# Kernel optimization log

Hardware: AMD Instinct MI355X
Metric: run time of the kernel (lower is better)

## Reference

```python
import jax, jax.numpy as jnp
import numpy as np

WS = 7          # window size (square)
SS = 3          # shift size
NH = 6          # num heads
EPS = 1e-5      # LayerNorm eps (torch default)


def _ln(x, g, b):
    m = jnp.mean(x, axis=-1, keepdims=True)
    v = jnp.mean(jnp.square(x - m), axis=-1, keepdims=True)
    return (x - m) * jax.lax.rsqrt(v + EPS) * g + b


def _window_partition(x):
    # (B,H,W,C) -> (B*nW, WS*WS, C)
    B, H, W, C = x.shape
    x = x.reshape(B, H // WS, WS, W // WS, WS, C)
    return x.transpose(0, 1, 3, 2, 4, 5).reshape(-1, WS * WS, C)


def _window_reverse(w, B, H, W):
    C = w.shape[-1]
    x = w.reshape(B, H // WS, W // WS, WS, WS, C)
    return x.transpose(0, 1, 3, 2, 4, 5).reshape(B, H, W, C)


def _make_rpi():
    coords = np.stack(np.meshgrid(np.arange(WS), np.arange(WS), indexing='ij'))  # (2,WS,WS)
    cf = coords.reshape(2, -1)
    rel = cf[:, :, None] - cf[:, None, :]            # (2,N,N)
    rel = rel.transpose(1, 2, 0).astype(np.int64)
    rel[..., 0] += WS - 1
    rel[..., 1] += WS - 1
    rel[..., 0] *= 2 * WS - 1
    return rel.sum(-1)                               # (N,N)


def _make_mask(H, W):
    # standard shifted-window attention mask, values in {0, -100}
    img = np.zeros((H, W), dtype=np.float32)
    cnt = 0
    for hs in (slice(0, -WS), slice(-WS, -SS), slice(-SS, None)):
        for ws_ in (slice(0, -WS), slice(-WS, -SS), slice(-SS, None)):
            img[hs, ws_] = cnt
            cnt += 1
    win = img.reshape(H // WS, WS, W // WS, WS).transpose(0, 2, 1, 3).reshape(-1, WS * WS)
    diff = win[:, None, :] - win[:, :, None]
    return np.where(diff != 0, np.float32(-100.0), np.float32(0.0))  # (nW,N,N)


def setup_inputs() -> dict:
    key = jax.random.key(0)
    ks = jax.random.split(key, 8)
    B, H, W, C = 16, 112, 112, 192
    Dh = C * 4
    s = 0.02
    inp = {
        'x': jax.random.normal(ks[0], (B, H, W, C), jnp.float32),
        'mask_matrix': jnp.asarray(_make_mask(H, W)),
        'rpi': jnp.asarray(_make_rpi(), jnp.int32),
        'rpb_table': s * jax.random.normal(ks[1], ((2 * WS - 1) ** 2, NH), jnp.float32),
        'norm1_g': jnp.ones((C,), jnp.float32),
        'norm1_b': jnp.zeros((C,), jnp.float32),
        'qkv_w': s * jax.random.normal(ks[2], (3 * C, C), jnp.float32),
        'qkv_b': jnp.zeros((3 * C,), jnp.float32),
        'proj_w': s * jax.random.normal(ks[3], (C, C), jnp.float32),
        'proj_b': jnp.zeros((C,), jnp.float32),
        'norm2_g': jnp.ones((C,), jnp.float32),
        'norm2_b': jnp.zeros((C,), jnp.float32),
        'fc1_w': s * jax.random.normal(ks[4], (Dh, C), jnp.float32),
        'fc1_b': jnp.zeros((Dh,), jnp.float32),
        'fc2_w': s * jax.random.normal(ks[5], (C, Dh), jnp.float32),
        'fc2_b': jnp.zeros((C,), jnp.float32),
    }
    return inp


def reference(x, mask_matrix, rpi, rpb_table, norm1_g, norm1_b, qkv_w, qkv_b,
              proj_w, proj_b, norm2_g, norm2_b, fc1_w, fc1_b, fc2_w, fc2_b):
    B, H, W, C = x.shape
    N = WS * WS
    hd = C // NH
    scale = hd ** -0.5

    shortcut = x
    xn = _ln(x, norm1_g, norm1_b)
    shifted = jnp.roll(xn, shift=(-SS, -SS), axis=(1, 2))

    xw = _window_partition(shifted)                          # (B_, N, C)
    B_ = xw.shape[0]
    qkv = xw @ qkv_w.T + qkv_b                               # (B_, N, 3C)
    qkv = qkv.reshape(B_, N, 3, NH, hd).transpose(2, 0, 3, 1, 4)
    q, k, v = qkv[0] * scale, qkv[1], qkv[2]                 # (B_, NH, N, hd)

    attn = jnp.einsum('bhnd,bhmd->bhnm', q, k)               # (B_, NH, N, N)
    bias = rpb_table[rpi.reshape(-1)].reshape(N, N, NH).transpose(2, 0, 1)
    attn = attn + bias[None]

    nW = mask_matrix.shape[0]
    attn = attn.reshape(B_ // nW, nW, NH, N, N) + mask_matrix[None, :, None]
    attn = jax.nn.softmax(attn.reshape(B_, NH, N, N), axis=-1)

    out = jnp.einsum('bhnm,bhmd->bhnd', attn, v)             # (B_, NH, N, hd)
    out = out.transpose(0, 2, 1, 3).reshape(B_, N, C)
    out = out @ proj_w.T + proj_b

    shifted = _window_reverse(out, B, H, W)
    xa = jnp.roll(shifted, shift=(SS, SS), axis=(1, 2))
    x = shortcut + xa

    h = _ln(x, norm2_g, norm2_b)
    h = jax.nn.gelu(h @ fc1_w.T + fc1_b, approximate=False)
    h = h @ fc2_w.T + fc2_b
    return x + h
```

## Files before the change

kernel.cpp:

```cpp
#include <hip/hip_runtime.h>
#include <hip/hip_bf16.h>

typedef __hip_bfloat16 bf16;
typedef __attribute__((ext_vector_type(8))) short bh8;
typedef __attribute__((ext_vector_type(4))) short bh4;
typedef __attribute__((ext_vector_type(4))) float f4;

#define TOKENS 200704
#define CDIM   192

__device__ __forceinline__ void gload16(const bf16* g, bf16* l) {
    __builtin_amdgcn_global_load_lds((const __attribute__((address_space(1))) void*)g,
                                     (__attribute__((address_space(3))) void*)l,
                                     16, 0, 0);
}
#define MFMA __builtin_amdgcn_mfma_f32_16x16x32_bf16

__device__ __forceinline__ void stv(float* p, float v) { *p = v; }
__device__ __forceinline__ void stv(bf16* p, float v)  { *p = __float2bfloat16(v); }
__device__ __forceinline__ short f2bs(float v) {
    bf16 h = __float2bfloat16(v); return *(short*)&h;
}

__device__ __forceinline__ int row2tok(int row) {
    int win = row / 49, n = row - win * 49;
    int b = win >> 8, rem = win & 255;
    int hs = (rem >> 4) * 7 + n / 7;
    int wsx = (rem & 15) * 7 + n % 7;
    int hh = hs + 3; if (hh >= 112) hh -= 112;
    int ww = wsx + 3; if (ww >= 112) ww -= 112;
    return (b * 112 + hh) * 112 + ww;
}

__global__ void cvt_all(const float* __restrict__ a, const float* __restrict__ b,
                        const float* __restrict__ c, const float* __restrict__ d,
                        bf16* __restrict__ dst) {
    int i = blockIdx.x * 256 + threadIdx.x;
    if (i >= 442368) return;
    float v;
    if (i < 110592)       v = a[i];
    else if (i < 147456)  v = b[i - 110592];
    else if (i < 294912)  v = c[i - 147456];
    else                  v = d[i - 294912];
    dst[i] = __float2bfloat16(v);
}

__global__ void bmp_kernel(const int* __restrict__ rpi, const float* __restrict__ tab,
                           const float* __restrict__ mask, float* __restrict__ bmp) {
    int idx = blockIdx.x * 256 + threadIdx.x;
    if (idx >= 98304) return;
    int cls = idx / 24576, rem = idx - cls * 24576;
    int h = rem >> 12, qk = rem & 4095;
    int qq = qk >> 6, kk = qk & 63;
    float v;
    if (kk >= 49) v = -1e30f;
    else if (qq >= 49) v = 0.f;
    else {
        int rep = ((cls & 2) ? 240 : 0) + ((cls & 1) ? 15 : 0);
        v = tab[rpi[qq * 49 + kk] * 6 + h] + mask[rep * 2401 + qq * 49 + kk];
    }
    bmp[idx] = v;
}

template<int GATHER>
__global__ __launch_bounds__(256)
void ln_kernel(const float* __restrict__ src, const float* __restrict__ gw,
               const float* __restrict__ bw, bf16* __restrict__ dst) {
    const int lane = threadIdx.x & 63;
    const int gwv  = (blockIdx.x * 256 + threadIdx.x) >> 6;
    const int nwv  = (gridDim.x * 256) >> 6;
    const float g0 = gw[lane], g1 = gw[lane + 64], g2 = gw[lane + 128];
    const float b0 = bw[lane], b1 = bw[lane + 64], b2 = bw[lane + 128];
    for (int row = gwv; row < TOKENS; row += nwv) {
        const float* p = GATHER ? src + (size_t)row2tok(row) * CDIM
                                : src + (size_t)row * CDIM;
        float v0 = p[lane], v1 = p[lane + 64], v2 = p[lane + 128];
        float s = v0 + v1 + v2;
        float q = v0 * v0 + v1 * v1 + v2 * v2;
        #pragma unroll
        for (int o = 32; o; o >>= 1) { s += __shfl_xor(s, o, 64); q += __shfl_xor(q, o, 64); }
        float mean = s * (1.f / 192.f);
        float var  = q * (1.f / 192.f) - mean * mean;
        float rstd = rsqrtf(var + 1e-5f);
        bf16* d = dst + (size_t)row * CDIM;
        d[lane]       = __float2bfloat16((v0 - mean) * rstd * g0 + b0);
        d[lane + 64]  = __float2bfloat16((v1 - mean) * rstd * g1 + b1);
        d[lane + 128] = __float2bfloat16((v2 - mean) * rstd * g2 + b2);
    }
}

template<int EPI, int FUSELN, typename OutT>
__global__ __launch_bounds__(256)
void gemm_bt(const bf16* __restrict__ A, const bf16* __restrict__ W,
             const float* __restrict__ bias, OutT* out,
             const float* res, int N, int K,
             const float* __restrict__ g2, const float* __restrict__ b2g,
             bf16* __restrict__ hbuf) {
    __shared__ __align__(16) bf16 As[128 * 32];
    __shared__ __align__(16) bf16 Bs[192 * 32];
    __shared__ float rsum[FUSELN ? 128 : 1][2], rsq[FUSELN ? 128 : 1][2];
    const int tid = threadIdx.x, wid = tid >> 6, lane = tid & 63;
    const int mbase = blockIdx.y * 128, nbase = blockIdx.x * 192;
    const int wm = wid >> 1, wn = wid & 1;
    const int r = lane & 15, q = lane >> 4;
    const int sx = (q ^ ((r >> 1) & 3)) << 3;
    const bf16* Ab = A + (size_t)mbase * K;
    const bf16* Wb = W + (size_t)nbase * K;
    f4 acc[4][6] = {};
    const int cbase = wid * 64 + lane;
    for (int k0 = 0; k0 < K; k0 += 32) {
        #pragma unroll
        for (int p = 0; p < 2; ++p) {
            int ci = p * 256 + cbase;
            int row = ci >> 2, g = (ci & 3) ^ ((row >> 1) & 3);
            gload16(Ab + (size_t)row * K + (k0 + (g << 3)),
                    &As[(p * 256 + wid * 64) * 8]);
        }
        #pragma unroll
        for (int p = 0; p < 3; ++p) {
            int ci = p * 256 + cbase;
            int row = ci >> 2, g = (ci & 3) ^ ((row >> 1) & 3);
            gload16(Wb + (size_t)row * K + (k0 + (g << 3)),
                    &Bs[(p * 256 + wid * 64) * 8]);
        }
        __syncthreads();
        bh8 af[4], bfr[6];
        #pragma unroll
        for (int i = 0; i < 4; ++i)
            af[i] = *(const bh8*)&As[(wm * 64 + i * 16 + r) * 32 + sx];
        #pragma unroll
        for (int j = 0; j < 6; ++j)
            bfr[j] = *(const bh8*)&Bs[(wn * 96 + j * 16 + r) * 32 + sx];
        #pragma unroll
        for (int i = 0; i < 4; ++i)
            #pragma unroll
            for (int j = 0; j < 6; ++j)
                acc[i][j] = MFMA(af[i], bfr[j], acc[i][j], 0, 0, 0);
        __syncthreads();
    }
    const int cr = q, cc = r;
    if constexpr (EPI == 0) {
        #pragma unroll
        for (int i = 0; i < 4; ++i)
            #pragma unroll
            for (int j = 0; j < 6; ++j) {
                int ncol = nbase + wn * 96 + j * 16 + cc;
                float bv = bias[ncol];
                #pragma unroll
                for (int rr = 0; rr < 4; ++rr) {
                    int row = mbase + wm * 64 + i * 16 + cr * 4 + rr;
                    stv(&out[(size_t)row * N + ncol], acc[i][j][rr] + bv);
                }
            }
    } else {
        #pragma unroll
        for (int i = 0; i < 4; ++i) {
            size_t dstRow[4];
            float ps[4], pq[4];
            #pragma unroll
            for (int rr = 0; rr < 4; ++rr) {
                int row = mbase + wm * 64 + i * 16 + cr * 4 + rr;
                dstRow[rr] = (size_t)row2tok(row) * CDIM;
                ps[rr] = 0.f; pq[rr] = 0.f;
            }
            #pragma unroll
            for (int j = 0; j < 6; ++j) {
                int ncol = nbase + wn * 96 + j * 16 + cc;
                float bv = bias[ncol];
                #pragma unroll
                for (int rr = 0; rr < 4; ++rr) {
                    float v = acc[i][j][rr] + bv + res[dstRow[rr] + ncol];
                    stv(&out[dstRow[rr] + ncol], v);
                    acc[i][j][rr] = v;
                    ps[rr] += v; pq[rr] += v * v;
                }
            }
            if constexpr (FUSELN) {
                #pragma unroll
                for (int rr = 0; rr < 4; ++rr) {
                    float s = ps[rr], qq = pq[rr];
                    #pragma unroll
                    for (int o = 1; o < 16; o <<= 1) { s += __shfl_xor(s, o, 64); qq += __shfl_xor(qq, o, 64); }
                    if (cc == 0) {
                        int rl = wm * 64 + i * 16 + cr * 4 + rr;
                        rsum[rl][wn] = s; rsq[rl][wn] = qq;
                    }
                }
            }
        }
        if constexpr (FUSELN) {
            __syncthreads();
            #pragma unroll
            for (int i = 0; i < 4; ++i) {
                size_t dstRow[4];
                float mean[4], rstd[4];
                #pragma unroll
                for (int rr = 0; rr < 4; ++rr) {
                    int rl = wm * 64 + i * 16 + cr * 4 + rr;
                    dstRow[rr] = (size_t)row2tok(mbase + rl) * CDIM;
                    float m = (rsum[rl][0] + rsum[rl][1]) * (1.f / 192.f);
                    float var = (rsq[rl][0] + rsq[rl][1]) * (1.f / 192.f) - m * m;
                    mean[rr] = m; rstd[rr] = rsqrtf(var + 1e-5f);
                }
                #pragma unroll
                for (int j = 0; j < 6; ++j) {
                    int ncol = nbase + wn * 96 + j * 16 + cc;
                    float gv = g2[ncol], bvv = b2g[ncol];
                    #pragma unroll
                    for (int rr = 0; rr < 4; ++rr)
                        hbuf[dstRow[rr] + ncol] =
                            __float2bfloat16((acc[i][j][rr] - mean[rr]) * rstd[rr] * gv + bvv);
                }
            }
        }
    }
}

__global__ __launch_bounds__(384, 3)
void qkvattn_kernel(const bf16* __restrict__ xw, const bf16* __restrict__ wq,
                    const float* __restrict__ qkvb, const float* __restrict__ bmp,
                    bf16* __restrict__ attno) {
    __shared__ __align__(16) bf16 xs[2][64][32];
    __shared__ __align__(16) bf16 qk[6][2][64][32];
    __shared__ __align__(16) bf16 vt[6][32][64];
    const int tid = threadIdx.x, h = tid >> 6, lane = tid & 63;
    const int r = lane & 15, q = lane >> 4;
    const int win = blockIdx.x;
    const int sxk = (q ^ ((r >> 1) & 3)) << 3;

    f4 aqk[4][4] = {}, av[4][2] = {};
    if (tid < 256) {
        int tok = tid >> 2, kg = (tid & 3) ^ ((tok >> 1) & 3);
        int srow = win * 49 + tok; if (srow > 200703) srow = 200703;
        gload16(xw + (size_t)srow * 192 + kg * 8, &xs[0][0][0] + tid * 8);
    }
    __syncthreads();
    for (int ks = 0; ks < 6; ++ks) {
        const int buf = ks & 1;
        if (ks < 5 && tid < 256) {
            int tok = tid >> 2, kg = (tid & 3) ^ ((tok >> 1) & 3);
            int srow = win * 49 + tok; if (srow > 200703) srow = 200703;
            gload16(xw + (size_t)srow * 192 + (ks + 1) * 32 + kg * 8,
                    &xs[buf ^ 1][0][0] + tid * 8);
        }
        bh8 wqk[4], wv[2], xf[4];
        #pragma unroll
        for (int i = 0; i < 4; ++i)
            wqk[i] = *(const bh8*)&wq[(size_t)((i >> 1) * 192 + h * 32 + (i & 1) * 16 + r) * 192 + ks * 32 + q * 8];
        #pragma unroll
        for (int jv = 0; jv < 2; ++jv)
            wv[jv] = *(const bh8*)&wq[(size_t)(384 + h * 32 + jv * 16 + r) * 192 + ks * 32 + q * 8];
        #pragma unroll
        for (int mt = 0; mt < 4; ++mt)
            xf[mt] = *(const bh8*)&xs[buf][mt * 16 + r][sxk];
        #pragma unroll
        for (int i = 0; i < 4; ++i)
            #pragma unroll
            for (int jn = 0; jn < 4; ++jn)
                aqk[i][jn] = MFMA(wqk[i], xf[jn], aqk[i][jn], 0, 0, 0);
        #pragma unroll
        for (int mt = 0; mt < 4; ++mt)
            #pragma unroll
            for (int jv = 0; jv < 2; ++jv)
                av[mt][jv] = MFMA(xf[mt], wv[jv], av[mt][jv], 0, 0, 0);
        __syncthreads();
    }
    bf16* qkh = &qk[h][0][0][0];
    #pragma unroll
    for (int i = 0; i < 4; ++i) {
        const int t = i >> 1;
        const f4 bz = *(const f4*)&qkvb[t * 192 + h * 32 + (i & 1) * 16 + q * 4];
        const float sc = (i < 2) ? 0.17677669529663689f : 1.0f;
        #pragma unroll
        for (int jn = 0; jn < 4; ++jn) {
            const int tok = jn * 16 + r;
            bh4 w;
            #pragma unroll
            for (int rr = 0; rr < 4; ++rr)
                w[rr] = f2bs((aqk[i][jn][rr] + bz[rr]) * sc);
            const int g = (((i & 1) * 4 + q) ^ ((tok & 3) << 1));
            *(bh4*)&qkh[(t * 64 + tok) * 32 + g * 4] = w;
        }
    }
    bf16* vth = &vt[h][0][0];
    #pragma unroll
    for (int jv = 0; jv < 2; ++jv) {
        const float bv = qkvb[384 + h * 32 + jv * 16 + r];
        const int d = jv * 16 + r;
        #pragma unroll
        for (int mt = 0; mt < 4; ++mt) {
            bh4 w;
            #pragma unroll
            for (int rr = 0; rr < 4; ++rr)
                w[rr] = f2bs(av[mt][jv][rr] + bv);
            const int g = ((mt * 4 + q) ^ ((r & 7) << 1));
            *(bh4*)&vth[d * 64 + g * 4] = w;
        }
    }
    f4 as[4][4] = {};
    {
        const int sl = ((2 * q) ^ ((r & 3) << 1)) << 2;
        bh8 kf[4], qf[4];
        #pragma unroll
        for (int mt = 0; mt < 4; ++mt)
            kf[mt] = *(const bh8*)&qkh[(64 + mt * 16 + r) * 32 + sl];
        #pragma unroll
        for (int jn = 0; jn < 4; ++jn)
            qf[jn] = *(const bh8*)&qkh[(jn * 16 + r) * 32 + sl];
        #pragma unroll
        for (int mt = 0; mt < 4; ++mt)
            #pragma unroll
            for (int jn = 0; jn < 4; ++jn)
                as[mt][jn] = MFMA(kf[mt], qf[jn], as[mt][jn], 0, 0, 0);
    }
    const int rem = win & 255;
    const int cls = (((rem >> 4) == 15) ? 2 : 0) + (((rem & 15) == 15) ? 1 : 0);
    const float* bmh = bmp + ((size_t)(cls * 6 + h) << 12);
    #pragma unroll
    for (int jn = 0; jn < 4; ++jn) {
        const int qq = jn * 16 + r;
        #pragma unroll
        for (int mt = 0; mt < 4; ++mt) {
            const f4 b = *(const f4*)&bmh[qq * 64 + mt * 16 + q * 4];
            #pragma unroll
            for (int rr = 0; rr < 4; ++rr) as[mt][jn][rr] += b[rr];
        }
    }
    float inv4[4];
    #pragma unroll
    for (int jn = 0; jn < 4; ++jn) {
        float mx = -1e30f;
        #pragma unroll
        for (int mt = 0; mt < 4; ++mt)
            #pragma unroll
            for (int rr = 0; rr < 4; ++rr) mx = fmaxf(mx, as[mt][jn][rr]);
        mx = fmaxf(mx, __shfl_xor(mx, 16, 64));
        mx = fmaxf(mx, __shfl_xor(mx, 32, 64));
        float sm = 0.f;
        #pragma unroll
        for (int mt = 0; mt < 4; ++mt)
            #pragma unroll
            for (int rr = 0; rr < 4; ++rr) {
                float e = __expf(as[mt][jn][rr] - mx);
                as[mt][jn][rr] = e; sm += e;
            }
        sm += __shfl_xor(sm, 16, 64);
        sm += __shfl_xor(sm, 32, 64);
        inv4[jn] = 1.f / sm;
    }
    #pragma unroll
    for (int jn = 0; jn < 4; ++jn) {
        const int qq = jn * 16 + r;
        #pragma unroll
        for (int mt = 0; mt < 4; ++mt) {
            bh4 w;
            #pragma unroll
            for (int rr = 0; rr < 4; ++rr) w[rr] = f2bs(as[mt][jn][rr] * inv4[jn]);
            const int g = ((mt * 4 + q) ^ ((r & 7) << 1));
            *(bh4*)&qkh[qq * 64 + g * 4] = w;
        }
    }
    f4 ao[4][2] = {};
    #pragma unroll
    for (int k2 = 0; k2 < 2; ++k2) {
        const int sl = ((k2 * 8 + 2 * q) ^ ((r & 7) << 1)) << 2;
        bh8 pf[4], vf[2];
        #pragma unroll
        for (int mt = 0; mt < 4; ++mt)
            pf[mt] = *(const bh8*)&qkh[(mt * 16 + r) * 64 + sl];
        #pragma unroll
        for (int jv = 0; jv < 2; ++jv)
            vf[jv] = *(const bh8*)&vth[(jv * 16 + r) * 64 + sl];
        #pragma unroll
        for (int mt = 0; mt < 4; ++mt)
            #pragma unroll
            for (int jv = 0; jv < 2; ++jv)
                ao[mt][jv] = MFMA(pf[mt], vf[jv], ao[mt][jv], 0, 0, 0);
    }
    #pragma unroll
    for (int mt = 0; mt < 4; ++mt)
        #pragma unroll
        for (int jv = 0; jv < 2; ++jv) {
            const int d = jv * 16 + r;
            #pragma unroll
            for (int rr = 0; rr < 4; ++rr) {
                const int qq = mt * 16 + q * 4 + rr;
                if (qq < 49)
                    attno[((size_t)win * 49 + qq) * 192 + h * 32 + d] =
                        __float2bfloat16(ao[mt][jv][rr]);
            }
        }
}

__global__ __launch_bounds__(256, 4)
void mlp_kernel(const bf16* __restrict__ Aht, const bf16* __restrict__ w1,
                const float* __restrict__ b1, const bf16* __restrict__ w2,
                const float* __restrict__ b2, float* __restrict__ out) {
    __shared__ __align__(16) bf16 As[6][64][32];
    __shared__ __align__(16) bf16 Hs[2][64][64];
    const int tid = threadIdx.x, wid = tid >> 6, lane = tid & 63;
    const int mbase = blockIdx.x * 64;
    const int r = lane & 15, q = lane >> 4, ko = q * 8;
    const int sxA = (q ^ ((r >> 1) & 3)) << 3;
    #pragma unroll
    for (int it = 0; it < 6; ++it) {
        int l = it * 256 + wid * 64 + lane;
        int ks = l >> 8, rem2 = l & 255, row = rem2 >> 2;
        int g = (rem2 & 3) ^ ((row >> 1) & 3);
        gload16(Aht + (size_t)(mbase + row) * 192 + ks * 32 + g * 8,
                &As[0][0][0] + (size_t)(it * 256 + wid * 64) * 8);
    }
    __syncthreads();
    f4 acc2[4][3] = {};
    for (int c = 0; c < 12; ++c) {
        const int cb = c * 64;
        bh8 w1f[6];
        #pragma unroll
        for (int ks = 0; ks < 6; ++ks)
            w1f[ks] = *(const bh8*)&w1[(size_t)(cb + wid * 16 + r) * 192 + ks * 32 + ko];
        f4 acc1[4] = {};
        #pragma unroll
        for (int ks = 0; ks < 6; ++ks)
            #pragma unroll
            for (int i = 0; i < 4; ++i) {
                bh8 af = *(const bh8*)(&As[ks][0][0] + (i * 16 + r) * 32 + sxA);
                acc1[i] = MFMA(af, w1f[ks], acc1[i], 0, 0, 0);
            }
        bh8 w2f[2][3];
        #pragma unroll
        for (int k2 = 0; k2 < 2; ++k2)
            #pragma unroll
            for (int j = 0; j < 3; ++j)
                w2f[k2][j] = *(const bh8*)&w2[(size_t)(wid * 48 + j * 16 + r) * 768 + cb + k2 * 32 + ko];
        const float b1v = b1[cb + wid * 16 + r];
        bf16 (*Hp)[64] = Hs[c & 1];
        #pragma unroll
        for (int i = 0; i < 4; ++i) {
            #pragma unroll
            for (int rr = 0; rr < 4; ++rr) {
                int row = i * 16 + q * 4 + rr;
                int col = wid * 16 + r;
                float v = acc1[i][rr] + b1v;
                float u = v * (1.5957691216f + 0.0713548162f * v * v);
                float e = __expf(u);
                Hp[row][(((col >> 3) ^ (row & 7)) << 3) | (col & 7)] =
                    __float2bfloat16(v * e / (e + 1.f));
            }
        }
        __syncthreads();
        #pragma unroll
        for (int k2 = 0; k2 < 2; ++k2)
            #pragma unroll
            for (int i = 0; i < 4; ++i) {
                int row = i * 16 + r;
                bh8 af = *(const bh8*)(&Hp[row][0] + ((((k2 * 4 + q) ^ (row & 7)) & 7) << 3));
                #pragma unroll
                for (int j = 0; j < 3; ++j)
                    acc2[i][j] = MFMA(af, w2f[k2][j], acc2[i][j], 0, 0, 0);
            }
    }
    #pragma unroll
    for (int i = 0; i < 4; ++i)
        #pragma unroll
        for (int j = 0; j < 3; ++j) {
            int ncol = wid * 48 + j * 16 + r;
            float bv = b2[ncol];
            #pragma unroll
            for (int rr = 0; rr < 4; ++rr) {
                size_t idx = (size_t)(mbase + i * 16 + q * 4 + rr) * 192 + ncol;
                out[idx] = acc2[i][j][rr] + bv + out[idx];
            }
        }
}

extern "C" void kernel_launch(void* const* d_in, const int* in_sizes, int n_in,
                              void* d_out, int out_size, void* d_ws, size_t ws_size,
                              hipStream_t stream) {
    const float* x     = (const float*)d_in[0];
    const float* mask  = (const float*)d_in[1];
    const int*   rpi   = (const int*)d_in[2];
    const float* rpb   = (const float*)d_in[3];
    const float* n1g   = (const float*)d_in[4];
    const float* n1b   = (const float*)d_in[5];
    const float* qkvw  = (const float*)d_in[6];
    const float* qkvb  = (const float*)d_in[7];
    const float* projw = (const float*)d_in[8];
    const float* projb = (const float*)d_in[9];
    const float* n2g   = (const float*)d_in[10];
    const float* n2b   = (const float*)d_in[11];
    const float* fc1w  = (const float*)d_in[12];
    const float* fc1b  = (const float*)d_in[13];
    const float* fc2w  = (const float*)d_in[14];
    const float* fc2b  = (const float*)d_in[15];

    char* ws = (char*)d_ws;
    bf16*  attno  = (bf16*)ws;
    float* bmp    = (float*)(ws + 77070336);
    bf16*  wq     = (bf16*)(ws + 77463552);
    bf16*  wp     = (bf16*)(ws + 77684736);
    bf16*  w1     = (bf16*)(ws + 77758464);
    bf16*  w2     = (bf16*)(ws + 78053376);
    bf16*  xw     = (bf16*)d_out;
    float* x1     = (float*)d_out;

    const bool fuse = ws_size >= 155418624ull;
    bf16* hbuf = fuse ? (bf16*)(ws + 78348288) : (bf16*)ws;

    cvt_all<<<1728, 256, 0, stream>>>(qkvw, projw, fc1w, fc2w, wq);
    bmp_kernel<<<384, 256, 0, stream>>>(rpi, rpb, mask, bmp);

    ln_kernel<1><<<2048, 256, 0, stream>>>(x, n1g, n1b, xw);
    qkvattn_kernel<<<4096, 384, 0, stream>>>(xw, wq, qkvb, bmp, attno);
    if (fuse) {
        gemm_bt<1, 1, float><<<dim3(1, 1568), 256, 0, stream>>>(
            attno, wp, projb, x1, x, 192, 192, n2g, n2b, hbuf);
    } else {
        gemm_bt<1, 0, float><<<dim3(1, 1568), 256, 0, stream>>>(
            attno, wp, projb, x1, x, 192, 192, nullptr, nullptr, nullptr);
        ln_kernel<0><<<2048, 256, 0, stream>>>(x1, n2g, n2b, hbuf);
    }
    mlp_kernel<<<3136, 256, 0, stream>>>(hbuf, w1, fc1b, w2, fc2b, (float*)d_out);
}
```

Measured before the change: 737.0 us.

## Fuse output projection, residual add and LayerNorm2 into the attention kernel

```diff
diff --git a/kernel.cpp b/kernel.cpp
--- a/kernel.cpp
+++ b/kernel.cpp
@@ -89,16 +89,13 @@
     }
 }
 
-template<int EPI, int FUSELN, typename OutT>
+template<int EPI, typename OutT>
 __global__ __launch_bounds__(256)
 void gemm_bt(const bf16* __restrict__ A, const bf16* __restrict__ W,
              const float* __restrict__ bias, OutT* out,
-             const float* res, int N, int K,
-             const float* __restrict__ g2, const float* __restrict__ b2g,
-             bf16* __restrict__ hbuf) {
+             const float* res, int N, int K) {
     __shared__ __align__(16) bf16 As[128 * 32];
     __shared__ __align__(16) bf16 Bs[192 * 32];
-    __shared__ float rsum[FUSELN ? 128 : 1][2], rsq[FUSELN ? 128 : 1][2];
     const int tid = threadIdx.x, wid = tid >> 6, lane = tid & 63;
     const int mbase = blockIdx.y * 128, nbase = blockIdx.x * 192;
     const int wm = wid >> 1, wn = wid & 1;
@@ -139,87 +136,38 @@
         __syncthreads();
     }
     const int cr = q, cc = r;
-    if constexpr (EPI == 0) {
-        #pragma unroll
-        for (int i = 0; i < 4; ++i)
-            #pragma unroll
-            for (int j = 0; j < 6; ++j) {
-                int ncol = nbase + wn * 96 + j * 16 + cc;
-                float bv = bias[ncol];
-                #pragma unroll
-                for (int rr = 0; rr < 4; ++rr) {
-                    int row = mbase + wm * 64 + i * 16 + cr * 4 + rr;
-                    stv(&out[(size_t)row * N + ncol], acc[i][j][rr] + bv);
-                }
-            }
-    } else {
-        #pragma unroll
-        for (int i = 0; i < 4; ++i) {
-            size_t dstRow[4];
-            float ps[4], pq[4];
+    #pragma unroll
+    for (int i = 0; i < 4; ++i) {
+        size_t dstRow[4];
+        #pragma unroll
+        for (int rr = 0; rr < 4; ++rr) {
+            int row = mbase + wm * 64 + i * 16 + cr * 4 + rr;
+            dstRow[rr] = (EPI == 1) ? (size_t)row2tok(row) * CDIM : (size_t)row * N;
+        }
+        #pragma unroll
+        for (int j = 0; j < 6; ++j) {
+            int ncol = nbase + wn * 96 + j * 16 + cc;
+            float bv = bias[ncol];
             #pragma unroll
             for (int rr = 0; rr < 4; ++rr) {
-                int row = mbase + wm * 64 + i * 16 + cr * 4 + rr;
-                dstRow[rr] = (size_t)row2tok(row) * CDIM;
-                ps[rr] = 0.f; pq[rr] = 0.f;
-            }
-            #pragma unroll
-            for (int j = 0; j < 6; ++j) {
-                int ncol = nbase + wn * 96 + j * 16 + cc;
-                float bv = bias[ncol];
-                #pragma unroll
-                for (int rr = 0; rr < 4; ++rr) {
-                    float v = acc[i][j][rr] + bv + res[dstRow[rr] + ncol];
-                    stv(&out[dstRow[rr] + ncol], v);
-                    acc[i][j][rr] = v;
-                    ps[rr] += v; pq[rr] += v * v;
-                }
-            }
-            if constexpr (FUSELN) {
-                #pragma unroll
-                for (int rr = 0; rr < 4; ++rr) {
-                    float s = ps[rr], qq = pq[rr];
-                    #pragma unroll
-                    for (int o = 1; o < 16; o <<= 1) { s += __shfl_xor(s, o, 64); qq += __shfl_xor(qq, o, 64); }
-                    if (cc == 0) {
-                        int rl = wm * 64 + i * 16 + cr * 4 + rr;
-                        rsum[rl][wn] = s; rsq[rl][wn] = qq;
-                    }
-                }
-            }
-        }
-        if constexpr (FUSELN) {
-            __syncthreads();
-            #pragma unroll
-            for (int i = 0; i < 4; ++i) {
-                size_t dstRow[4];
-                float mean[4], rstd[4];
-                #pragma unroll
-                for (int rr = 0; rr < 4; ++rr) {
-                    int rl = wm * 64 + i * 16 + cr * 4 + rr;
-                    dstRow[rr] = (size_t)row2tok(mbase + rl) * CDIM;
-                    float m = (rsum[rl][0] + rsum[rl][1]) * (1.f / 192.f);
-                    float var = (rsq[rl][0] + rsq[rl][1]) * (1.f / 192.f) - m * m;
-                    mean[rr] = m; rstd[rr] = rsqrtf(var + 1e-5f);
-                }
-                #pragma unroll
-                for (int j = 0; j < 6; ++j) {
-                    int ncol = nbase + wn * 96 + j * 16 + cc;
-                    float gv = g2[ncol], bvv = b2g[ncol];
-                    #pragma unroll
-                    for (int rr = 0; rr < 4; ++rr)
-                        hbuf[dstRow[rr] + ncol] =
-                            __float2bfloat16((acc[i][j][rr] - mean[rr]) * rstd[rr] * gv + bvv);
-                }
-            }
-        }
-    }
-}
-
+                float v = acc[i][j][rr] + bv;
+                size_t di = dstRow[rr] + ncol;
+                if constexpr (EPI == 1) v += res[di];
+                stv(&out[di], v);
+            }
+        }
+    }
+}
+
+template<int PROJ>
 __global__ __launch_bounds__(384, 3)
 void qkvattn_kernel(const bf16* __restrict__ xw, const bf16* __restrict__ wq,
                     const float* __restrict__ qkvb, const float* __restrict__ bmp,
-                    bf16* __restrict__ attno) {
+                    bf16* __restrict__ attno,
+                    const bf16* __restrict__ wp, const float* __restrict__ projb,
+                    const float* __restrict__ xres, float* __restrict__ x1,
+                    const float* __restrict__ g2, const float* __restrict__ b2g,
+                    bf16* __restrict__ hbuf) {
     __shared__ __align__(16) bf16 xs[2][64][32];
     __shared__ __align__(16) bf16 qk[6][2][64][32];
     __shared__ __align__(16) bf16 vt[6][32][64];
@@ -346,7 +294,7 @@
             }
         sm += __shfl_xor(sm, 16, 64);
         sm += __shfl_xor(sm, 32, 64);
-        inv4[jn] = 1.f / sm;
+        inv4[jn] = __builtin_amdgcn_rcpf(sm);
     }
     #pragma unroll
     for (int jn = 0; jn < 4; ++jn) {
@@ -377,19 +325,126 @@
             for (int jv = 0; jv < 2; ++jv)
                 ao[mt][jv] = MFMA(pf[mt], vf[jv], ao[mt][jv], 0, 0, 0);
     }
+    if constexpr (!PROJ) {
+        #pragma unroll
+        for (int mt = 0; mt < 4; ++mt)
+            #pragma unroll
+            for (int jv = 0; jv < 2; ++jv) {
+                const int d = jv * 16 + r;
+                #pragma unroll
+                for (int rr = 0; rr < 4; ++rr) {
+                    const int qq = mt * 16 + q * 4 + rr;
+                    if (qq < 49)
+                        attno[((size_t)win * 49 + qq) * 192 + h * 32 + d] =
+                            __float2bfloat16(ao[mt][jv][rr]);
+                }
+            }
+        return;
+    } else {
+    __syncthreads();
+    bf16* Os = &qk[0][0][0][0];
+    #pragma unroll
+    for (int jv = 0; jv < 2; ++jv) {
+        const int col = h * 32 + jv * 16 + r;
+        const int gc = col >> 3, cl = col & 7;
+        #pragma unroll
+        for (int mt = 0; mt < 4; ++mt)
+            #pragma unroll
+            for (int rr = 0; rr < 4; ++rr) {
+                const int row = mt * 16 + q * 4 + rr;
+                Os[row * 192 + ((gc ^ ((row >> 1) & 3)) << 3) + cl] =
+                    __float2bfloat16(ao[mt][jv][rr]);
+            }
+    }
+    __syncthreads();
+    f4 pr[4][2] = {};
+    #pragma unroll
+    for (int ks = 0; ks < 6; ++ks) {
+        bh8 wpf[2];
+        #pragma unroll
+        for (int jv = 0; jv < 2; ++jv)
+            wpf[jv] = *(const bh8*)&wp[(size_t)(h * 32 + jv * 16 + r) * 192 + ks * 32 + q * 8];
+        const int kg = ks * 4 + q;
+        #pragma unroll
+        for (int mt = 0; mt < 4; ++mt) {
+            const int row = mt * 16 + r;
+            bh8 of = *(const bh8*)&Os[row * 192 + ((kg ^ ((row >> 1) & 3)) << 3)];
+            #pragma unroll
+            for (int jv = 0; jv < 2; ++jv)
+                pr[mt][jv] = MFMA(of, wpf[jv], pr[mt][jv], 0, 0, 0);
+        }
+    }
+    float pbv[2], g2v[2], b2v[2];
+    #pragma unroll
+    for (int jv = 0; jv < 2; ++jv) {
+        const int col = h * 32 + jv * 16 + r;
+        pbv[jv] = projb[col]; g2v[jv] = g2[col]; b2v[jv] = b2g[col];
+    }
+    int tokm[4][4];
     #pragma unroll
     for (int mt = 0; mt < 4; ++mt)
         #pragma unroll
+        for (int rr = 0; rr < 4; ++rr) {
+            int grow = win * 49 + mt * 16 + q * 4 + rr;
+            if (grow > 200703) grow = 200703;
+            tokm[mt][rr] = row2tok(grow);
+        }
+    #pragma unroll
+    for (int mt = 0; mt < 4; ++mt)
+        #pragma unroll
         for (int jv = 0; jv < 2; ++jv) {
-            const int d = jv * 16 + r;
+            const int col = h * 32 + jv * 16 + r;
             #pragma unroll
             for (int rr = 0; rr < 4; ++rr) {
                 const int qq = mt * 16 + q * 4 + rr;
-                if (qq < 49)
-                    attno[((size_t)win * 49 + qq) * 192 + h * 32 + d] =
-                        __float2bfloat16(ao[mt][jv][rr]);
-            }
-        }
+                const size_t di = (size_t)tokm[mt][rr] * 192 + col;
+                float v = pr[mt][jv][rr] + pbv[jv] + xres[di];
+                pr[mt][jv][rr] = v;
+                if (qq < 49) x1[di] = v;
+            }
+        }
+    float* rs = (float*)&xs[0][0][0];
+    float* rq = rs + 512;
+    float* mr = rs + 1024;
+    #pragma unroll
+    for (int mt = 0; mt < 4; ++mt)
+        #pragma unroll
+        for (int rr = 0; rr < 4; ++rr) {
+            float s = pr[mt][0][rr] + pr[mt][1][rr];
+            float sq = pr[mt][0][rr] * pr[mt][0][rr] + pr[mt][1][rr] * pr[mt][1][rr];
+            #pragma unroll
+            for (int o = 1; o < 16; o <<= 1) { s += __shfl_xor(s, o, 64); sq += __shfl_xor(sq, o, 64); }
+            if (r == 0) {
+                const int row = mt * 16 + q * 4 + rr;
+                rs[row * 8 + h] = s; rq[row * 8 + h] = sq;
+            }
+        }
+    __syncthreads();
+    if (tid < 64) {
+        float s = 0.f, sq = 0.f;
+        #pragma unroll
+        for (int h6 = 0; h6 < 6; ++h6) { s += rs[tid * 8 + h6]; sq += rq[tid * 8 + h6]; }
+        float m = s * (1.f / 192.f);
+        float var = sq * (1.f / 192.f) - m * m;
+        mr[tid * 2] = m; mr[tid * 2 + 1] = rsqrtf(var + 1e-5f);
+    }
+    __syncthreads();
+    #pragma unroll
+    for (int mt = 0; mt < 4; ++mt)
+        #pragma unroll
+        for (int rr = 0; rr < 4; ++rr) {
+            const int qq = mt * 16 + q * 4 + rr;
+            if (qq < 49) {
+                const float m = mr[qq * 2], rstd = mr[qq * 2 + 1];
+                #pragma unroll
+                for (int jv = 0; jv < 2; ++jv) {
+                    const int col = h * 32 + jv * 16 + r;
+                    hbuf[(size_t)tokm[mt][rr] * 192 + col] =
+                        __float2bfloat16((pr[mt][jv][rr] - m) * rstd * g2v[jv] + b2v[jv]);
+                }
+            }
+        }
+    }
 }
 
 __global__ __launch_bounds__(256, 4)
@@ -442,9 +497,10 @@
                 int col = wid * 16 + r;
                 float v = acc1[i][rr] + b1v;
                 float u = v * (1.5957691216f + 0.0713548162f * v * v);
-                float e = __expf(u);
+                float en = __expf(-u);
+                float t = __builtin_amdgcn_rcpf(1.f + en);
                 Hp[row][(((col >> 3) ^ (row & 7)) << 3) | (col & 7)] =
-                    __float2bfloat16(v * e / (e + 1.f));
+                    __float2bfloat16(v * t);
             }
         }
         __syncthreads();
@@ -494,30 +550,43 @@
     const float* fc2b  = (const float*)d_in[15];
 
     char* ws = (char*)d_ws;
-    bf16*  attno  = (bf16*)ws;
-    float* bmp    = (float*)(ws + 77070336);
-    bf16*  wq     = (bf16*)(ws + 77463552);
-    bf16*  wp     = (bf16*)(ws + 77684736);
-    bf16*  w1     = (bf16*)(ws + 77758464);
-    bf16*  w2     = (bf16*)(ws + 78053376);
-    bf16*  xw     = (bf16*)d_out;
-    float* x1     = (float*)d_out;
-
     const bool fuse = ws_size >= 155418624ull;
-    bf16* hbuf = fuse ? (bf16*)(ws + 78348288) : (bf16*)ws;
-
-    cvt_all<<<1728, 256, 0, stream>>>(qkvw, projw, fc1w, fc2w, wq);
-    bmp_kernel<<<384, 256, 0, stream>>>(rpi, rpb, mask, bmp);
-
-    ln_kernel<1><<<2048, 256, 0, stream>>>(x, n1g, n1b, xw);
-    qkvattn_kernel<<<4096, 384, 0, stream>>>(xw, wq, qkvb, bmp, attno);
+
     if (fuse) {
-        gemm_bt<1, 1, float><<<dim3(1, 1568), 256, 0, stream>>>(
-            attno, wp, projb, x1, x, 192, 192, n2g, n2b, hbuf);
+        bf16*  xw    = (bf16*)ws;
+        bf16*  hbuf  = (bf16*)(ws + 77070336);
+        float* bmp   = (float*)(ws + 154140672);
+        bf16*  wq    = (bf16*)(ws + 154533888);
+        bf16*  wp    = (bf16*)(ws + 154755072);
+        bf16*  w1    = (bf16*)(ws + 154828800);
+        bf16*  w2    = (bf16*)(ws + 155123712);
+        float* x1    = (float*)d_out;
+
+        cvt_all<<<1728, 256, 0, stream>>>(qkvw, projw, fc1w, fc2w, wq);
+        bmp_kernel<<<384, 256, 0, stream>>>(rpi, rpb, mask, bmp);
+        ln_kernel<1><<<2048, 256, 0, stream>>>(x, n1g, n1b, xw);
+        qkvattn_kernel<1><<<4096, 384, 0, stream>>>(xw, wq, qkvb, bmp, nullptr,
+                                                    wp, projb, x, x1, n2g, n2b, hbuf);
+        mlp_kernel<<<3136, 256, 0, stream>>>(hbuf, w1, fc1b, w2, fc2b, (float*)d_out);
     } else {
-        gemm_bt<1, 0, float><<<dim3(1, 1568), 256, 0, stream>>>(
-            attno, wp, projb, x1, x, 192, 192, nullptr, nullptr, nullptr);
+        bf16*  attno = (bf16*)ws;
+        float* bmp   = (float*)(ws + 77070336);
+        bf16*  wq    = (bf16*)(ws + 77463552);
+        bf16*  wp    = (bf16*)(ws + 77684736);
+        bf16*  w1    = (bf16*)(ws + 77758464);
+        bf16*  w2    = (bf16*)(ws + 78053376);
+        bf16*  xw    = (bf16*)d_out;
+        float* x1    = (float*)d_out;
+        bf16*  hbuf  = (bf16*)ws;
+
+        cvt_all<<<1728, 256, 0, stream>>>(qkvw, projw, fc1w, fc2w, wq);
+        bmp_kernel<<<384, 256, 0, stream>>>(rpi, rpb, mask, bmp);
+        ln_kernel<1><<<2048, 256, 0, stream>>>(x, n1g, n1b, xw);
+        qkvattn_kernel<0><<<4096, 384, 0, stream>>>(xw, wq, qkvb, bmp, attno,
+                                                    nullptr, nullptr, nullptr, nullptr,
+                                                    nullptr, nullptr, nullptr);
+        gemm_bt<1, float><<<dim3(1, 1568), 256, 0, stream>>>(attno, wp, projb, x1, x, 192, 192);
         ln_kernel<0><<<2048, 256, 0, stream>>>(x1, n2g, n2b, hbuf);
-    }
-    mlp_kernel<<<3136, 256, 0, stream>>>(hbuf, w1, fc1b, w2, fc2b, (float*)d_out);
-}
+        mlp_kernel<<<3136, 256, 0, stream>>>(hbuf, w1, fc1b, w2, fc2b, (float*)d_out);
+    }
+}
```

Result: slower. 893.0 us (+21.2%).

## Preload full x tile into LDS and drop per-step syncs in qkv-attention kernel

Applied to the files above, without the earlier changes.

```diff
diff --git a/kernel.cpp b/kernel.cpp
--- a/kernel.cpp
+++ b/kernel.cpp
@@ -216,33 +216,29 @@
     }
 }
 
-__global__ __launch_bounds__(384, 3)
+__global__ __launch_bounds__(384, 2)
 void qkvattn_kernel(const bf16* __restrict__ xw, const bf16* __restrict__ wq,
                     const float* __restrict__ qkvb, const float* __restrict__ bmp,
                     bf16* __restrict__ attno) {
-    __shared__ __align__(16) bf16 xs[2][64][32];
+    __shared__ __align__(16) bf16 xsf[6][64][32];
     __shared__ __align__(16) bf16 qk[6][2][64][32];
-    __shared__ __align__(16) bf16 vt[6][32][64];
     const int tid = threadIdx.x, h = tid >> 6, lane = tid & 63;
     const int r = lane & 15, q = lane >> 4;
     const int win = blockIdx.x;
     const int sxk = (q ^ ((r >> 1) & 3)) << 3;
 
+    #pragma unroll
+    for (int it = 0; it < 4; ++it) {
+        int l = it * 384 + tid;
+        int ks = l >> 8, rem = l & 255, tok = rem >> 2;
+        int kg = (rem & 3) ^ ((tok >> 1) & 3);
+        int srow = win * 49 + tok; if (srow > 200703) srow = 200703;
+        gload16(xw + (size_t)srow * 192 + ks * 32 + kg * 8,
+                &xsf[0][0][0] + (size_t)l * 8);
+    }
+    __syncthreads();
     f4 aqk[4][4] = {}, av[4][2] = {};
-    if (tid < 256) {
-        int tok = tid >> 2, kg = (tid & 3) ^ ((tok >> 1) & 3);
-        int srow = win * 49 + tok; if (srow > 200703) srow = 200703;
-        gload16(xw + (size_t)srow * 192 + kg * 8, &xs[0][0][0] + tid * 8);
-    }
-    __syncthreads();
     for (int ks = 0; ks < 6; ++ks) {
-        const int buf = ks & 1;
-        if (ks < 5 && tid < 256) {
-            int tok = tid >> 2, kg = (tid & 3) ^ ((tok >> 1) & 3);
-            int srow = win * 49 + tok; if (srow > 200703) srow = 200703;
-            gload16(xw + (size_t)srow * 192 + (ks + 1) * 32 + kg * 8,
-                    &xs[buf ^ 1][0][0] + tid * 8);
-        }
         bh8 wqk[4], wv[2], xf[4];
         #pragma unroll
         for (int i = 0; i < 4; ++i)
@@ -252,7 +248,7 @@
             wv[jv] = *(const bh8*)&wq[(size_t)(384 + h * 32 + jv * 16 + r) * 192 + ks * 32 + q * 8];
         #pragma unroll
         for (int mt = 0; mt < 4; ++mt)
-            xf[mt] = *(const bh8*)&xs[buf][mt * 16 + r][sxk];
+            xf[mt] = *(const bh8*)&xsf[ks][mt * 16 + r][sxk];
         #pragma unroll
         for (int i = 0; i < 4; ++i)
             #pragma unroll
@@ -263,8 +259,8 @@
             #pragma unroll
             for (int jv = 0; jv < 2; ++jv)
                 av[mt][jv] = MFMA(xf[mt], wv[jv], av[mt][jv], 0, 0, 0);
-        __syncthreads();
-    }
+    }
+    __syncthreads();
     bf16* qkh = &qk[h][0][0][0];
     #pragma unroll
     for (int i = 0; i < 4; ++i) {
@@ -282,7 +278,7 @@
             *(bh4*)&qkh[(t * 64 + tok) * 32 + g * 4] = w;
         }
     }
-    bf16* vth = &vt[h][0][0];
+    bf16* vth = &xsf[0][0][0] + h * 2048;
     #pragma unroll
     for (int jv = 0; jv < 2; ++jv) {
         const float bv = qkvb[384 + h * 32 + jv * 16 + r];
@@ -346,7 +342,7 @@
             }
         sm += __shfl_xor(sm, 16, 64);
         sm += __shfl_xor(sm, 32, 64);
-        inv4[jn] = 1.f / sm;
+        inv4[jn] = __builtin_amdgcn_rcpf(sm);
     }
     #pragma unroll
     for (int jn = 0; jn < 4; ++jn) {
@@ -442,9 +438,10 @@
                 int col = wid * 16 + r;
                 float v = acc1[i][rr] + b1v;
                 float u = v * (1.5957691216f + 0.0713548162f * v * v);
-                float e = __expf(u);
+                float en = __expf(-u);
+                float t = __builtin_amdgcn_rcpf(1.f + en);
                 Hp[row][(((col >> 3) ^ (row & 7)) << 3) | (col & 7)] =
-                    __float2bfloat16(v * e / (e + 1.f));
+                    __float2bfloat16(v * t);
             }
         }
         __syncthreads();
```

New measurement: 731.3 us. About the same (-0.8%).
